# Kernel optimization log

Measured on AMD Instinct MI355X. Metric: run time of the kernel, lower is better.

Reference implementation:

```python
import jax, jax.numpy as jnp
import numpy as np

GROUP_SIZE = 64

def setup_inputs() -> dict:
    key = jax.random.key(0)
    ks = jax.random.split(key, 7)
    T, N, K, NG = 4096, 4096, 11264, 4096 // GROUP_SIZE
    x = jax.random.normal(ks[0], (T, N), dtype=jnp.float32)
    Q = jax.random.randint(ks[1], (K, N), 0, 8, dtype=jnp.int32)  # uint8 3-bit codes
    scales = jax.random.uniform(ks[2], (K, NG), dtype=jnp.float32)
    zeros = jax.random.uniform(ks[3], (K, NG), dtype=jnp.float32) * 7.0
    mu1 = jax.random.uniform(ks[4], (N,), dtype=jnp.float32) + 0.5
    mu2 = jax.random.uniform(ks[5], (K,), dtype=jnp.float32) + 0.5
    bias = jax.random.normal(ks[6], (K,), dtype=jnp.float32)
    return {"x": x, "Q": Q, "scales": scales, "zeros": zeros, "mu1": mu1, "mu2": mu2, "bias": bias}

def reference(x, Q, scales, zeros, mu1, mu2, bias):
    K, N = Q.shape
    ng = scales.shape[1]
    # group-wise dequant: (Q - zero) * scale, groups along N
    Qg = Q.astype(jnp.float32).reshape(K, ng, GROUP_SIZE)
    W_deq_norm = ((Qg - zeros[:, :, None]) * scales[:, :, None]).reshape(K, N)
    # Sinkhorn mu rescale: per-row mu2, per-column mu1
    W_deq = W_deq_norm * mu2[:, None] * mu1[None, :]
    out = x @ W_deq.T + bias
    return out
```

## Files before the change

### kernel.cpp

```cpp
#include <hip/hip_runtime.h>
#include <stdint.h>
#include <stddef.h>


typedef __attribute__((ext_vector_type(8))) short bfrag;
typedef __attribute__((ext_vector_type(4))) float f32x4;
typedef __attribute__((ext_vector_type(4))) int   i32x4;

__device__ __forceinline__ short f2bf(float f) {
    uint32_t u = __float_as_uint(f);
    u += 0x7fffu + ((u >> 16) & 1u);
    return (short)(u >> 16);
}

__device__ __forceinline__ void gload_lds16(const void* g, void* l) {
    __builtin_amdgcn_global_load_lds(
        (const __attribute__((address_space(1))) void*)g,
        (__attribute__((address_space(3))) void*)l,
        16, 0, 0);
}

__global__ void cvt_x_kernel(const float* __restrict__ x, short* __restrict__ xb) {
    int i = blockIdx.x * 256 + threadIdx.x;
    const f32x4* xv = (const f32x4*)x;
    f32x4 a = xv[2 * i];
    f32x4 b = xv[2 * i + 1];
    bfrag o;
    o[0] = f2bf(a[0]); o[1] = f2bf(a[1]); o[2] = f2bf(a[2]); o[3] = f2bf(a[3]);
    o[4] = f2bf(b[0]); o[5] = f2bf(b[1]); o[6] = f2bf(b[2]); o[7] = f2bf(b[3]);
    ((bfrag*)xb)[i] = o;
}

__global__ void deq_w_kernel(const int* __restrict__ Q,
                             const float* __restrict__ scales,
                             const float* __restrict__ zeros,
                             const float* __restrict__ mu1,
                             const float* __restrict__ mu2,
                             short* __restrict__ wb,
                             int k0, int N, int NG) {
    int kl = blockIdx.y;
    int kg = k0 + kl;
    int c  = blockIdx.x * 256 + threadIdx.x;
    int n0 = c << 3;
    int g  = n0 >> 6;
    float s = scales[(size_t)kg * NG + g] * mu2[kg];
    float z = zeros[(size_t)kg * NG + g];
    const i32x4* qv = (const i32x4*)(Q + (size_t)kg * N + n0);
    i32x4 q0 = qv[0];
    i32x4 q1 = qv[1];
    const f32x4* uv = (const f32x4*)(mu1 + n0);
    f32x4 u0 = uv[0];
    f32x4 u1 = uv[1];
    bfrag o;
    o[0] = f2bf(((float)q0[0] - z) * s * u0[0]);
    o[1] = f2bf(((float)q0[1] - z) * s * u0[1]);
    o[2] = f2bf(((float)q0[2] - z) * s * u0[2]);
    o[3] = f2bf(((float)q0[3] - z) * s * u0[3]);
    o[4] = f2bf(((float)q1[0] - z) * s * u1[0]);
    o[5] = f2bf(((float)q1[1] - z) * s * u1[1]);
    o[6] = f2bf(((float)q1[2] - z) * s * u1[2]);
    o[7] = f2bf(((float)q1[3] - z) * s * u1[3]);
    ((bfrag*)wb)[(size_t)kl * (N >> 3) + c] = o;
}

#define BM 128
#define BN 128
#define BK 32

__global__ void gemm_bt_kernel(const short* __restrict__ A,
                               const short* __restrict__ B,
                               const float* __restrict__ bias,
                               float* __restrict__ C,
                               int Kc, int Nout, int col0) {
    __shared__ __attribute__((aligned(16))) short As[BM * BK];
    __shared__ __attribute__((aligned(16))) short Bs[BN * BK];

    const int tid  = threadIdx.x;
    const int lane = tid & 63;
    const int wave = tid >> 6;
    const int wm   = (wave >> 1) * 64;
    const int wn   = (wave & 1) * 64;
    const int bm   = blockIdx.y * BM;
    const int bnl  = blockIdx.x * BN;

    f32x4 acc[4][4];
#pragma unroll
    for (int i = 0; i < 4; i++)
#pragma unroll
        for (int j = 0; j < 4; j++)
            acc[i][j] = (f32x4){0.f, 0.f, 0.f, 0.f};

    const short* gA  = A + (size_t)(bm + (tid >> 2)) * Kc + (tid & 3) * 8;
    const short* gA2 = gA + (size_t)64 * Kc;
    const short* gB  = B + (size_t)(bnl + (tid >> 2)) * Kc + (tid & 3) * 8;
    const short* gB2 = gB + (size_t)64 * Kc;
    short* lA  = As + tid * 8;
    short* lA2 = As + 2048 + tid * 8;
    short* lB  = Bs + tid * 8;
    short* lB2 = Bs + 2048 + tid * 8;

    const int r  = lane & 15;
    const int ko = (lane >> 4) * 8;
    const short* pa = As + (wm + r) * BK + ko;
    const short* pb = Bs + (wn + r) * BK + ko;

    for (int k0 = 0; k0 < Kc; k0 += BK) {
        gload_lds16(gA + k0, lA);
        gload_lds16(gA2 + k0, lA2);
        gload_lds16(gB + k0, lB);
        gload_lds16(gB2 + k0, lB2);
        __syncthreads();

        bfrag af[4], bfv[4];
#pragma unroll
        for (int i = 0; i < 4; i++) af[i]  = *(const bfrag*)(pa + i * 16 * BK);
#pragma unroll
        for (int j = 0; j < 4; j++) bfv[j] = *(const bfrag*)(pb + j * 16 * BK);

#pragma unroll
        for (int i = 0; i < 4; i++)
#pragma unroll
            for (int j = 0; j < 4; j++)
                acc[i][j] = __builtin_amdgcn_mfma_f32_16x16x32_bf16(
                    af[i], bfv[j], acc[i][j], 0, 0, 0);

        __syncthreads();
    }

    const int row0  = bm + wm + (lane >> 4) * 4;
    const int colg0 = col0 + bnl + wn;
#pragma unroll
    for (int j = 0; j < 4; j++) {
        int col  = colg0 + j * 16 + r;
        float bv = bias[col];
#pragma unroll
        for (int i = 0; i < 4; i++) {
            int row = row0 + i * 16;
#pragma unroll
            for (int q = 0; q < 4; q++)
                C[(size_t)(row + q) * Nout + col] = acc[i][j][q] + bv;
        }
    }
}

__global__ void naive_kernel(const float* __restrict__ x, const int* __restrict__ Q,
                             const float* __restrict__ scales, const float* __restrict__ zeros,
                             const float* __restrict__ mu1, const float* __restrict__ mu2,
                             const float* __restrict__ bias, float* __restrict__ out,
                             int T, int N, int K, int NG) {
    long long total = (long long)T * K;
    for (long long idx = blockIdx.x * 256ll + threadIdx.x; idx < total;
         idx += (long long)gridDim.x * 256ll) {
        int t = (int)(idx / K);
        int k = (int)(idx - (long long)t * K);
        float s = 0.f;
        for (int n = 0; n < N; n++) {
            int g = n >> 6;
            float w = ((float)Q[(size_t)k * N + n] - zeros[(size_t)k * NG + g]) *
                      scales[(size_t)k * NG + g];
            s += x[(size_t)t * N + n] * w * mu1[n];
        }
        out[idx] = s * mu2[k] + bias[k];
    }
}

extern "C" void kernel_launch(void* const* d_in, const int* in_sizes, int n_in,
                              void* d_out, int out_size, void* d_ws, size_t ws_size,
                              hipStream_t stream) {
    const float* x      = (const float*)d_in[0];
    const int*   Q      = (const int*)d_in[1];
    const float* scales = (const float*)d_in[2];
    const float* zeros  = (const float*)d_in[3];
    const float* mu1    = (const float*)d_in[4];
    const float* mu2    = (const float*)d_in[5];
    const float* bias   = (const float*)d_in[6];
    float* out = (float*)d_out;

    const int N  = in_sizes[4];
    const int K  = in_sizes[5];
    const int T  = in_sizes[0] / N;
    const int NG = in_sizes[2] / K;

    const size_t xb_bytes  = (size_t)T * N * 2;
    const size_t row_bytes = (size_t)N * 2;

    if (ws_size < xb_bytes + 128 * row_bytes) {
        naive_kernel<<<4096, 256, 0, stream>>>(x, Q, scales, zeros, mu1, mu2,
                                               bias, out, T, N, K, NG);
        return;
    }

    short* xb = (short*)d_ws;
    short* wb = (short*)((char*)d_ws + xb_bytes);
    size_t max_rows = (ws_size - xb_bytes) / row_bytes;
    int CH = (int)((max_rows / 128) * 128);
    if (CH > K) CH = K;

    cvt_x_kernel<<<(T * N / 8) / 256, 256, 0, stream>>>(x, xb);

    for (int c0 = 0; c0 < K; c0 += CH) {
        int rows = (K - c0 < CH) ? (K - c0) : CH;
        dim3 dgrid(N / (8 * 256), rows);
        deq_w_kernel<<<dgrid, 256, 0, stream>>>(Q, scales, zeros, mu1, mu2, wb,
                                                c0, N, NG);
        dim3 ggrid(rows / BN, T / BM);
        gemm_bt_kernel<<<ggrid, 256, 0, stream>>>(xb, wb, bias, out, N, K, c0);
    }
}
```

Measured before the change: 797.4 us.

## Swizzle GEMM LDS layout, fold mu1 into x conversion, widen dequant threads

The LDS tile for A and B is now XOR-swizzled: global source columns are permuted at load time and the fragment reads apply the matching swizzle. This is meant to cut bank conflicts in the MFMA operand reads. The mu1 column scale moves from the weight dequant into the x-to-bf16 conversion, which is mathematically equivalent but changes where rounding happens. The dequant kernel now uses one block per row with 16 elements per thread and no longer reads mu1. The dequant launch assumes N/16 threads per block, so it only works while N is at most 16384.

```diff
diff --git a/kernel.cpp b/kernel.cpp
--- a/kernel.cpp
+++ b/kernel.cpp
@@ -20,47 +20,54 @@
         16, 0, 0);
 }
 
-__global__ void cvt_x_kernel(const float* __restrict__ x, short* __restrict__ xb) {
+__global__ void cvt_x_kernel(const float* __restrict__ x,
+                             const float* __restrict__ mu1,
+                             short* __restrict__ xb, int per ) {
     int i = blockIdx.x * 256 + threadIdx.x;
+    int cb = (i % per) * 8;
     const f32x4* xv = (const f32x4*)x;
     f32x4 a = xv[2 * i];
     f32x4 b = xv[2 * i + 1];
+    const f32x4* uv = (const f32x4*)(mu1 + cb);
+    f32x4 u0 = uv[0];
+    f32x4 u1 = uv[1];
     bfrag o;
-    o[0] = f2bf(a[0]); o[1] = f2bf(a[1]); o[2] = f2bf(a[2]); o[3] = f2bf(a[3]);
-    o[4] = f2bf(b[0]); o[5] = f2bf(b[1]); o[6] = f2bf(b[2]); o[7] = f2bf(b[3]);
+    o[0] = f2bf(a[0] * u0[0]); o[1] = f2bf(a[1] * u0[1]);
+    o[2] = f2bf(a[2] * u0[2]); o[3] = f2bf(a[3] * u0[3]);
+    o[4] = f2bf(b[0] * u1[0]); o[5] = f2bf(b[1] * u1[1]);
+    o[6] = f2bf(b[2] * u1[2]); o[7] = f2bf(b[3] * u1[3]);
     ((bfrag*)xb)[i] = o;
 }
 
 __global__ void deq_w_kernel(const int* __restrict__ Q,
                              const float* __restrict__ scales,
                              const float* __restrict__ zeros,
-                             const float* __restrict__ mu1,
                              const float* __restrict__ mu2,
                              short* __restrict__ wb,
                              int k0, int N, int NG) {
-    int kl = blockIdx.y;
+    int kl = blockIdx.x;
     int kg = k0 + kl;
-    int c  = blockIdx.x * 256 + threadIdx.x;
-    int n0 = c << 3;
+    int n0 = threadIdx.x << 4;
     int g  = n0 >> 6;
     float s = scales[(size_t)kg * NG + g] * mu2[kg];
     float z = zeros[(size_t)kg * NG + g];
     const i32x4* qv = (const i32x4*)(Q + (size_t)kg * N + n0);
-    i32x4 q0 = qv[0];
-    i32x4 q1 = qv[1];
-    const f32x4* uv = (const f32x4*)(mu1 + n0);
-    f32x4 u0 = uv[0];
-    f32x4 u1 = uv[1];
-    bfrag o;
-    o[0] = f2bf(((float)q0[0] - z) * s * u0[0]);
-    o[1] = f2bf(((float)q0[1] - z) * s * u0[1]);
-    o[2] = f2bf(((float)q0[2] - z) * s * u0[2]);
-    o[3] = f2bf(((float)q0[3] - z) * s * u0[3]);
-    o[4] = f2bf(((float)q1[0] - z) * s * u1[0]);
-    o[5] = f2bf(((float)q1[1] - z) * s * u1[1]);
-    o[6] = f2bf(((float)q1[2] - z) * s * u1[2]);
-    o[7] = f2bf(((float)q1[3] - z) * s * u1[3]);
-    ((bfrag*)wb)[(size_t)kl * (N >> 3) + c] = o;
+    bfrag* wv = (bfrag*)(wb + (size_t)kl * N + n0);
+#pragma unroll
+    for (int h = 0; h < 2; h++) {
+        i32x4 q0 = qv[2 * h];
+        i32x4 q1 = qv[2 * h + 1];
+        bfrag o;
+        o[0] = f2bf(((float)q0[0] - z) * s);
+        o[1] = f2bf(((float)q0[1] - z) * s);
+        o[2] = f2bf(((float)q0[2] - z) * s);
+        o[3] = f2bf(((float)q0[3] - z) * s);
+        o[4] = f2bf(((float)q1[0] - z) * s);
+        o[5] = f2bf(((float)q1[1] - z) * s);
+        o[6] = f2bf(((float)q1[2] - z) * s);
+        o[7] = f2bf(((float)q1[3] - z) * s);
+        wv[h] = o;
+    }
 }
 
 #define BM 128
@@ -90,9 +97,10 @@
         for (int j = 0; j < 4; j++)
             acc[i][j] = (f32x4){0.f, 0.f, 0.f, 0.f};
 
-    const short* gA  = A + (size_t)(bm + (tid >> 2)) * Kc + (tid & 3) * 8;
+    const int skc = ((tid & 3) ^ ((tid >> 3) & 3)) * 8;
+    const short* gA  = A + (size_t)(bm + (tid >> 2)) * Kc + skc;
     const short* gA2 = gA + (size_t)64 * Kc;
-    const short* gB  = B + (size_t)(bnl + (tid >> 2)) * Kc + (tid & 3) * 8;
+    const short* gB  = B + (size_t)(bnl + (tid >> 2)) * Kc + skc;
     const short* gB2 = gB + (size_t)64 * Kc;
     short* lA  = As + tid * 8;
     short* lA2 = As + 2048 + tid * 8;
@@ -100,9 +108,10 @@
     short* lB2 = Bs + 2048 + tid * 8;
 
     const int r  = lane & 15;
-    const int ko = (lane >> 4) * 8;
-    const short* pa = As + (wm + r) * BK + ko;
-    const short* pb = Bs + (wn + r) * BK + ko;
+    const int kc = lane >> 4;
+    const int sw = (kc ^ ((r >> 1) & 3)) * 8;
+    const short* pa = As + (wm + r) * BK + sw;
+    const short* pb = Bs + (wn + r) * BK + sw;
 
     for (int k0 = 0; k0 < Kc; k0 += BK) {
         gload_lds16(gA + k0, lA);
@@ -196,13 +205,12 @@
     int CH = (int)((max_rows / 128) * 128);
     if (CH > K) CH = K;
 
-    cvt_x_kernel<<<(T * N / 8) / 256, 256, 0, stream>>>(x, xb);
+    cvt_x_kernel<<<(T * N / 8) / 256, 256, 0, stream>>>(x, mu1, xb, N / 8);
 
     for (int c0 = 0; c0 < K; c0 += CH) {
         int rows = (K - c0 < CH) ? (K - c0) : CH;
-        dim3 dgrid(N / (8 * 256), rows);
-        deq_w_kernel<<<dgrid, 256, 0, stream>>>(Q, scales, zeros, mu1, mu2, wb,
-                                                c0, N, NG);
+        deq_w_kernel<<<rows, N / 16, 0, stream>>>(Q, scales, zeros, mu2, wb,
+                                                  c0, N, NG);
         dim3 ggrid(rows / BN, T / BM);
         gemm_bt_kernel<<<ggrid, 256, 0, stream>>>(xb, wb, bias, out, N, K, c0);
     }
```

New measurement: 804.2 us. No clear change (+0.8%).
